# Kernel tuning notes

Measured on AMD Instinct MI355X. Metric: run time of the kernel, lower is better.

## Reference

```python
import jax, jax.numpy as jnp
import numpy as np
from jax import lax

NUM_MASKS = 100
NUM_CLASSES = 81  # 80 + 1
KERNEL_DIM = 256
BIAS_PRIOR = float(-np.log((1 - 0.01) / 0.01))


def setup_inputs() -> dict:
    key = jax.random.key(0)
    ks = jax.random.split(key, 12)
    B, C, H, W = 4, 256, 160, 160
    D = C  # expand_dim = in_channels * num_groups
    inp = {
        "features": jax.random.normal(ks[0], (B, C, H, W), jnp.float32),
        # iam_conv: Conv2d(C, num_masks, 3, padding=1)
        "w_iam": jax.random.normal(ks[1], (NUM_MASKS, C, 3, 3), jnp.float32) * 0.01,
        "b_iam": jnp.full((NUM_MASKS,), BIAS_PRIOR, jnp.float32),
        "softmax_bias": jnp.ones((1,), jnp.float32),
        # fc: Linear(D, D), xavier-ish
        "w_fc": jax.random.normal(ks[2], (D, D), jnp.float32) * (1.0 / np.sqrt(D)),
        "b_fc": jnp.zeros((D,), jnp.float32),
        "w_cls": jax.random.normal(ks[3], (NUM_CLASSES, D), jnp.float32) * 0.01,
        "b_cls": jnp.full((NUM_CLASSES,), BIAS_PRIOR, jnp.float32),
        "w_ker": jax.random.normal(ks[4], (KERNEL_DIM, D), jnp.float32) * 0.01,
        "b_ker": jnp.zeros((KERNEL_DIM,), jnp.float32),
        "w_obj": jax.random.normal(ks[5], (1, D), jnp.float32) * (1.0 / np.sqrt(D)),
        "b_obj": jnp.zeros((1,), jnp.float32),
        "w_box": jax.random.normal(ks[6], (4, D), jnp.float32) * 0.01,
        "b_box": jnp.zeros((4,), jnp.float32),
    }
    return inp


def reference(features, w_iam, b_iam, softmax_bias, w_fc, b_fc,
              w_cls, b_cls, w_ker, b_ker, w_obj, b_obj, w_box, b_box):
    B, C, H, W = features.shape
    # conv score map: (B, num_masks, H, W)
    iam = lax.conv_general_dilated(
        features, w_iam, window_strides=(1, 1), padding="SAME",
        dimension_numbers=("NCHW", "OIHW", "NCHW")) + b_iam[None, :, None, None]
    # num_groups == 1: single group iam
    iam_flat = iam.reshape(B, NUM_MASKS, H * W)
    # softmax over HW with learned scalar bias (bias shifts uniformly -> no-op math-wise but kept faithful)
    iam_prob = jax.nn.softmax(iam_flat + softmax_bias[0], axis=-1)  # (B, M, HW)
    # spatial attention pooling: bmm(prob, feats^T) -> (B, M, C)
    inst = jnp.einsum("bmp,bcp->bmc", iam_prob, features.reshape(B, C, H * W))
    # prev_inst_features is None -> skip fc_fuse
    inst = jax.nn.relu(inst @ w_fc.T + b_fc)
    pred_logits = inst @ w_cls.T + b_cls
    pred_kernel = inst @ w_ker.T + b_ker
    pred_scores = inst @ w_obj.T + b_obj
    pred_bboxes = inst @ w_box.T + b_box
    return (pred_logits, pred_kernel, pred_scores, pred_bboxes, iam, inst)
```

## Files before the change

kernel.cpp:

```cpp
#include <hip/hip_runtime.h>
#include <hip/hip_bf16.h>

typedef __attribute__((ext_vector_type(8))) short bf16x8;
typedef __attribute__((ext_vector_type(4))) float f32x4;

#define HW_ 25600
#define HP_ 162
#define WP_ 162

__device__ __forceinline__ unsigned short f2bf(float f) {
    union { float f; unsigned u; } x; x.f = f;
    unsigned r = x.u + 0x7FFFu + ((x.u >> 16) & 1u);
    return (unsigned short)(r >> 16);
}
__device__ __forceinline__ float bf2f(unsigned short v) {
    union { unsigned u; float f; } x; x.u = ((unsigned)v) << 16;
    return x.f;
}

typedef const __attribute__((address_space(1))) unsigned int* gas_t;
typedef __attribute__((address_space(3))) unsigned int* las_t;
__device__ __forceinline__ void gl_lds16(const void* g, void* l) {
    __builtin_amdgcn_global_load_lds((gas_t)g, (las_t)l, 16, 0, 0);
}

__global__ __launch_bounds__(256) void k_prep(const float* __restrict__ w_iam,
                                              unsigned short* __restrict__ wp,
                                              unsigned short* __restrict__ fpad) {
    int bid = blockIdx.x;
    if (bid < 1152) {
        int idx = bid * 256 + threadIdx.x;
        int stage = idx >> 12;
        int r = idx & 4095;
        int m = r >> 5, cl = r & 31;
        int tap = stage >> 3, kc = stage & 7;
        int jj = (cl >> 3) ^ ((m >> 1) & 3);
        int c = kc * 32 + jj * 8 + (cl & 7);
        int dy = (tap * 11) >> 5, dx = tap - dy * 3;
        float v = (m < 100) ? w_iam[((m * 256 + c) * 3 + dy) * 3 + dx] : 0.f;
        wp[idx] = f2bf(v);
    } else {
        int idx = (bid - 1152) * 256 + threadIdx.x;
        const int perb = 164864;
        if (idx >= 4 * perb) return;
        int b = idx / perb;
        int r = idx - b * perb;
        int hp, wpp, c;
        if (r < 82944) {
            hp = (r < 41472) ? 0 : 161;
            int r2 = r % 41472;
            wpp = r2 >> 8; c = r2 & 255;
        } else {
            r -= 82944;
            wpp = (r < 40960) ? 0 : 161;
            int r2 = r % 40960;
            hp = 1 + (r2 >> 8); c = r2 & 255;
        }
        fpad[((b * HP_ + hp) * WP_ + wpp) * 256 + c] = 0;
    }
}

__global__ __launch_bounds__(256) void k_convert(const float* __restrict__ feat,
                                                 unsigned short* __restrict__ fpad) {
    int bid = blockIdx.x;
    int b = bid / 640;
    int h = (bid >> 2) % 160;
    int c0 = (bid & 3) * 64;
    __shared__ float tile[64][161];
    int t = threadIdx.x;
    const float4* src4 = (const float4*)(feat + ((long)(b * 256 + c0) * 160 + h) * 160);
    #pragma unroll
    for (int s = 0; s < 10; ++s) {
        int q = t + s * 256;
        int ci = q / 40;
        int w4 = q - ci * 40;
        float4 v = src4[(long)ci * 6400 + w4];
        tile[ci][w4 * 4 + 0] = v.x;
        tile[ci][w4 * 4 + 1] = v.y;
        tile[ci][w4 * 4 + 2] = v.z;
        tile[ci][w4 * 4 + 3] = v.w;
    }
    __syncthreads();
    int co = (t & 7) * 8, wq = t >> 3;
    unsigned short* dst = fpad + ((long)(b * HP_ + h + 1) * WP_ + 1) * 256 + c0 + co;
    #pragma unroll
    for (int wp = 0; wp < 5; ++wp) {
        int w = wq + wp * 32;
        bf16x8 v;
        #pragma unroll
        for (int j = 0; j < 8; ++j) v[j] = (short)f2bf(tile[co + j][w]);
        *(bf16x8*)(dst + (long)w * 256) = v;
    }
}

__global__ __launch_bounds__(256, 3) void k_conv(const unsigned short* __restrict__ fpad,
                                                 const unsigned short* __restrict__ wprep,
                                                 const float* __restrict__ b_iam,
                                                 float* __restrict__ iam) {
    int bid = blockIdx.x;
    bid = (bid & 7) * 100 + (bid >> 3);
    int b = bid / 200;
    int p0 = (bid % 200) * 128;
    int tid = threadIdx.x;
    int lane = tid & 63, wid = tid >> 6;
    int wr = wid >> 1, wc = wid & 1;

    __shared__ __align__(16) char smem[24576 + 2 * 8448];

    int h0 = p0 / 160, w0 = p0 - h0 * 160;
    int istar = 160 - w0;
    const unsigned short* fb = fpad + (long)b * HP_ * WP_ * 256;

    long rterm[2];
    {
        int c = tid & 3;
        #pragma unroll
        for (int i = 0; i < 2; ++i) {
            int r = i * 64 + (tid >> 2);
            rterm[i] = (long)r * 256 + ((c ^ ((r >> 1) & 3)) << 3);
        }
    }
    long rterm2;
    {
        int r = 128 + ((lane & 15) >> 2), c = lane & 3;
        rterm2 = (long)r * 256 + ((c ^ ((r >> 1) & 3)) << 3);
    }

    f32x4 acc[4][4];
    #pragma unroll
    for (int i = 0; i < 4; ++i)
        #pragma unroll
        for (int j = 0; j < 4; ++j)
            #pragma unroll
            for (int k = 0; k < 4; ++k) acc[i][j][k] = 0.f;

    int aBase = (wr << 12) + ((lane & 15) << 6) + ((((lane >> 4) ^ ((lane >> 1) & 3))) << 4);
    int rb[4];
    #pragma unroll
    for (int nf = 0; nf < 4; ++nf) {
        int i = wc * 64 + nf * 16 + (lane & 15);
        rb[nf] = i + 2 * (i >= istar);
    }

    auto issueA = [&](int s) {
        int dy = s >> 3, kc = s & 7;
        #pragma unroll
        for (int dx = 0; dx < 3; ++dx) {
            const unsigned short* ga = wprep + ((long)((dy * 3 + dx) * 8 + kc) << 12) + (tid << 3);
            char* Adst = smem + (dx << 13) + (wid << 10);
            gl_lds16(ga, Adst);
            gl_lds16(ga + 2048, Adst + 4096);
        }
    };
    auto issueB = [&](int s, int bi) {
        int dy = s >> 3, kc = s & 7;
        char* Bd = smem + 24576 + bi * 8448;
        long base = ((long)((h0 + dy) * WP_ + w0)) * 256 + (kc << 5);
        gl_lds16(fb + base + rterm[0], Bd + (wid << 10));
        gl_lds16(fb + base + rterm[1], Bd + 4096 + (wid << 10));
        if (lane < 16) gl_lds16(fb + base + rterm2, Bd + 8192);
    };

    auto compute = [&](int bi) {
        const char* Ab = smem;
        const char* Bb = smem + 24576 + bi * 8448;
        #pragma unroll
        for (int dx = 0; dx < 3; ++dx) {
            bf16x8 af[4], bfv[4];
            #pragma unroll
            for (int mf = 0; mf < 4; ++mf)
                af[mf] = *(const bf16x8*)(Ab + (dx << 13) + aBase + (mf << 10));
            #pragma unroll
            for (int nf = 0; nf < 4; ++nf) {
                int row = rb[nf] + dx;
                bfv[nf] = *(const bf16x8*)(Bb + (row << 6) +
                            ((((lane >> 4) ^ ((row >> 1) & 3))) << 4));
            }
            __builtin_amdgcn_s_setprio(1);
            #pragma unroll
            for (int mf = 0; mf < 4; ++mf)
                #pragma unroll
                for (int nf = 0; nf < 4; ++nf)
                    acc[mf][nf] = __builtin_amdgcn_mfma_f32_16x16x32_bf16(
                        af[mf], bfv[nf], acc[mf][nf], 0, 0, 0);
            __builtin_amdgcn_s_setprio(0);
        }
    };

    issueB(0, 0);
    issueA(0);
    for (int s = 0; s < 24; ++s) {
        if (s < 23) {
            issueB(s + 1, (s + 1) & 1);
            asm volatile("s_waitcnt vmcnt(3)" ::: "memory");
        } else {
            asm volatile("s_waitcnt vmcnt(0)" ::: "memory");
        }
        __builtin_amdgcn_sched_barrier(0);
        __builtin_amdgcn_s_barrier();
        __builtin_amdgcn_sched_barrier(0);
        compute(s & 1);
        __builtin_amdgcn_sched_barrier(0);
        __builtin_amdgcn_s_barrier();
        __builtin_amdgcn_sched_barrier(0);
        if (s < 23) issueA(s + 1);
    }

    float* dst = iam + (long)b * 100 * HW_;
    #pragma unroll
    for (int mf = 0; mf < 4; ++mf)
        #pragma unroll
        for (int nf = 0; nf < 4; ++nf) {
            int p = p0 + wc * 64 + nf * 16 + (lane & 15);
            int m0 = wr * 64 + mf * 16 + ((lane >> 4) << 2);
            #pragma unroll
            for (int j = 0; j < 4; ++j) {
                int m = m0 + j;
                if (m < 100) dst[(long)m * HW_ + p] = acc[mf][nf][j] + b_iam[m];
            }
        }
}

__global__ __launch_bounds__(256, 2) void k_pool(const float* __restrict__ feat,
                                                 const float* __restrict__ iam,
                                                 unsigned short* __restrict__ partials,
                                                 float* __restrict__ psum) {
    int bid = blockIdx.x;
    int b = bid / 100;
    int sl = bid - b * 100;
    int p0 = sl * 256;
    int tid = threadIdx.x, lane = tid & 63, wq = tid >> 6;

    __shared__ __align__(16) unsigned short A[128 * 72];
    __shared__ __align__(16) unsigned short Bl[256 * 72];
    __shared__ float sums[128];
    if (tid < 128) sums[tid] = 0.f;
    __syncthreads();

    f32x4 acc[7][4];
    #pragma unroll
    for (int i = 0; i < 7; ++i)
        #pragma unroll
        for (int j = 0; j < 4; ++j)
            #pragma unroll
            for (int k = 0; k < 4; ++k) acc[i][j][k] = 0.f;

    int kgrp = (lane >> 4) << 3;

    for (int ks = 0; ks < 4; ++ks) {
        int k0 = p0 + ks * 64;
        for (int s = 0; s < 4; ++s) {
            int q = tid + s * 256;
            int mi = q >> 3, j0 = (q & 7) * 8;
            bf16x8 o;
            if (mi < 100) {
                const float4* sp4 = (const float4*)(iam + (long)(b * 100 + mi) * HW_ + k0 + j0);
                float4 v0 = sp4[0], v1 = sp4[1];
                float xv[8] = {v0.x, v0.y, v0.z, v0.w, v1.x, v1.y, v1.z, v1.w};
                float ls = 0.f;
                #pragma unroll
                for (int j = 0; j < 8; ++j) {
                    float e = __expf(xv[j]);
                    o[j] = (short)f2bf(e);
                    ls += e;
                }
                atomicAdd(&sums[mi], ls);
            } else {
                #pragma unroll
                for (int j = 0; j < 8; ++j) o[j] = 0;
            }
            *(bf16x8*)(A + mi * 72 + j0) = o;
        }
        for (int s = 0; s < 8; ++s) {
            int q = tid + s * 256;
            int ci = q >> 3, j0 = (q & 7) * 8;
            const float4* sp4 = (const float4*)(feat + (long)(b * 256 + ci) * HW_ + k0 + j0);
            float4 v0 = sp4[0], v1 = sp4[1];
            float xv[8] = {v0.x, v0.y, v0.z, v0.w, v1.x, v1.y, v1.z, v1.w};
            bf16x8 o;
            #pragma unroll
            for (int j = 0; j < 8; ++j) o[j] = (short)f2bf(xv[j]);
            *(bf16x8*)(Bl + ci * 72 + j0) = o;
        }
        __syncthreads();
        #pragma unroll
        for (int kk = 0; kk < 64; kk += 32) {
            bf16x8 af[7], bfv[4];
            #pragma unroll
            for (int mf = 0; mf < 7; ++mf)
                af[mf] = *(const bf16x8*)(A + (mf * 16 + (lane & 15)) * 72 + kk + kgrp);
            #pragma unroll
            for (int nf = 0; nf < 4; ++nf)
                bfv[nf] = *(const bf16x8*)(Bl + (wq * 64 + nf * 16 + (lane & 15)) * 72 + kk + kgrp);
            #pragma unroll
            for (int mf = 0; mf < 7; ++mf)
                #pragma unroll
                for (int nf = 0; nf < 4; ++nf)
                    acc[mf][nf] = __builtin_amdgcn_mfma_f32_16x16x32_bf16(
                        af[mf], bfv[nf], acc[mf][nf], 0, 0, 0);
        }
        __syncthreads();
    }
    if (tid < 100) psum[(long)bid * 112 + tid] = sums[tid];
    unsigned short* dst = partials + (long)bid * 112 * 256;
    #pragma unroll
    for (int mf = 0; mf < 7; ++mf)
        #pragma unroll
        for (int nf = 0; nf < 4; ++nf) {
            int m0 = mf * 16 + ((lane >> 4) << 2);
            int c  = wq * 64 + nf * 16 + (lane & 15);
            #pragma unroll
            for (int j = 0; j < 4; ++j)
                dst[(long)(m0 + j) * 256 + c] = f2bf(acc[mf][nf][j]);
        }
}

__global__ __launch_bounds__(256) void k_redfc(const unsigned short* __restrict__ partials,
                                               const float* __restrict__ psum,
                                               const float* __restrict__ w_fc, const float* __restrict__ b_fc,
                                               const float* __restrict__ w_cls, const float* __restrict__ b_cls,
                                               const float* __restrict__ w_ker, const float* __restrict__ b_ker,
                                               const float* __restrict__ w_obj, const float* __restrict__ b_obj,
                                               const float* __restrict__ w_box, const float* __restrict__ b_box,
                                               float* __restrict__ out) {
    int r = blockIdx.x;
    int b = r / 100, m = r - b * 100;
    int t = threadIdx.x;
    __shared__ float red[256];
    __shared__ float row[256];
    __shared__ float inst_s[256];

    red[t] = (t < 100) ? psum[(long)(b * 100 + t) * 112 + m] : 0.f;
    __syncthreads();
    for (int o = 128; o > 0; o >>= 1) {
        if (t < o) red[t] += red[t + o];
        __syncthreads();
    }
    float d = red[0];

    float s = 0.f;
    for (int sl = 0; sl < 100; ++sl)
        s += bf2f(partials[((long)(b * 100 + sl) * 112 + m) * 256 + t]);
    row[t] = s / d;
    __syncthreads();
    {
        float acc = b_fc[t];
        const float4* wv = (const float4*)(w_fc + (long)t * 256);
        for (int c = 0; c < 64; ++c) {
            float4 w4 = wv[c];
            acc += w4.x * row[c * 4] + w4.y * row[c * 4 + 1] + w4.z * row[c * 4 + 2] + w4.w * row[c * 4 + 3];
        }
        acc = fmaxf(acc, 0.f);
        inst_s[t] = acc;
        out[10376800 + (long)r * 256 + t] = acc;
    }
    __syncthreads();
    {
        float acc = b_ker[t];
        const float4* wv = (const float4*)(w_ker + (long)t * 256);
        for (int c = 0; c < 64; ++c) {
            float4 w4 = wv[c];
            acc += w4.x * inst_s[c * 4] + w4.y * inst_s[c * 4 + 1] + w4.z * inst_s[c * 4 + 2] + w4.w * inst_s[c * 4 + 3];
        }
        out[32400 + (long)r * 256 + t] = acc;
    }
    if (t < 81) {
        float acc = b_cls[t];
        const float4* wv = (const float4*)(w_cls + (long)t * 256);
        for (int c = 0; c < 64; ++c) {
            float4 w4 = wv[c];
            acc += w4.x * inst_s[c * 4] + w4.y * inst_s[c * 4 + 1] + w4.z * inst_s[c * 4 + 2] + w4.w * inst_s[c * 4 + 3];
        }
        out[(long)r * 81 + t] = acc;
    }
    if (t == 0) {
        float acc = b_obj[0];
        for (int c = 0; c < 256; ++c) acc += w_obj[c] * inst_s[c];
        out[134800 + r] = acc;
    }
    if (t >= 1 && t < 5) {
        int j = t - 1;
        float acc = b_box[j];
        for (int c = 0; c < 256; ++c) acc += w_box[j * 256 + c] * inst_s[c];
        out[135200 + (long)r * 4 + j] = acc;
    }
}

extern "C" void kernel_launch(void* const* d_in, const int* in_sizes, int n_in,
                              void* d_out, int out_size, void* d_ws, size_t ws_size,
                              hipStream_t stream) {
    const float* feat  = (const float*)d_in[0];
    const float* w_iam = (const float*)d_in[1];
    const float* b_iam = (const float*)d_in[2];
    const float* w_fc  = (const float*)d_in[4];
    const float* b_fc  = (const float*)d_in[5];
    const float* w_cls = (const float*)d_in[6];
    const float* b_cls = (const float*)d_in[7];
    const float* w_ker = (const float*)d_in[8];
    const float* b_ker = (const float*)d_in[9];
    const float* w_obj = (const float*)d_in[10];
    const float* b_obj = (const float*)d_in[11];
    const float* w_box = (const float*)d_in[12];
    const float* b_box = (const float*)d_in[13];
    float* out = (float*)d_out;

    char* ws = (char*)d_ws;
    unsigned short* fpad  = (unsigned short*)ws;
    unsigned short* wprep = (unsigned short*)(ws + 53747712);
    float* iam = out + 136800;

    unsigned short* partials = (unsigned short*)ws;
    float* psum              = (float*)(ws + 22937600);

    k_prep   <<<dim3(3728), dim3(256), 0, stream>>>(w_iam, wprep, fpad);
    k_convert<<<dim3(2560), dim3(256), 0, stream>>>(feat, fpad);
    k_conv   <<<dim3(800),  dim3(256), 0, stream>>>(fpad, wprep, b_iam, iam);
    k_pool   <<<dim3(400),  dim3(256), 0, stream>>>(feat, iam, partials, psum);
    k_redfc  <<<dim3(400),  dim3(256), 0, stream>>>(partials, psum, w_fc, b_fc, w_cls, b_cls,
                                                    w_ker, b_ker, w_obj, b_obj, w_box, b_box, out);
}
```

Baseline: 191.6 us.

## Widen conv tile to 256 pixels with 8 waves and merge prep/convert kernels

The conv kernel now uses 512-thread blocks, each covering 256 output pixels instead of 128. The weight (A) tile is shared by twice as many pixel columns, which halves weight loads per output and halves the block count. The B halo now spans two row wraps, and the wait counts are split per wave. The weight-prep, pad-zeroing and feature-conversion kernels are also fused into one launch to save launch overhead, but the larger LDS footprint and block size may reduce occupancy.

Result: faster. 173.2 us (median of 3 runs) (-9.6%).

```diff
diff --git a/kernel.cpp b/kernel.cpp
--- a/kernel.cpp
+++ b/kernel.cpp
@@ -24,9 +24,10 @@
     __builtin_amdgcn_global_load_lds((gas_t)g, (las_t)l, 16, 0, 0);
 }
 
-__global__ __launch_bounds__(256) void k_prep(const float* __restrict__ w_iam,
-                                              unsigned short* __restrict__ wp,
-                                              unsigned short* __restrict__ fpad) {
+__global__ __launch_bounds__(256) void k_prepcvt(const float* __restrict__ w_iam,
+                                                 unsigned short* __restrict__ wp,
+                                                 const float* __restrict__ feat,
+                                                 unsigned short* __restrict__ fpad) {
     int bid = blockIdx.x;
     if (bid < 1152) {
         int idx = bid * 256 + threadIdx.x;
@@ -39,7 +40,7 @@
         int dy = (tap * 11) >> 5, dx = tap - dy * 3;
         float v = (m < 100) ? w_iam[((m * 256 + c) * 3 + dy) * 3 + dx] : 0.f;
         wp[idx] = f2bf(v);
-    } else {
+    } else if (bid < 3728) {
         int idx = (bid - 1152) * 256 + threadIdx.x;
         const int perb = 164864;
         if (idx >= 4 * perb) return;
@@ -57,73 +58,67 @@
             hp = 1 + (r2 >> 8); c = r2 & 255;
         }
         fpad[((b * HP_ + hp) * WP_ + wpp) * 256 + c] = 0;
-    }
-}
-
-__global__ __launch_bounds__(256) void k_convert(const float* __restrict__ feat,
-                                                 unsigned short* __restrict__ fpad) {
-    int bid = blockIdx.x;
-    int b = bid / 640;
-    int h = (bid >> 2) % 160;
-    int c0 = (bid & 3) * 64;
-    __shared__ float tile[64][161];
-    int t = threadIdx.x;
-    const float4* src4 = (const float4*)(feat + ((long)(b * 256 + c0) * 160 + h) * 160);
-    #pragma unroll
-    for (int s = 0; s < 10; ++s) {
-        int q = t + s * 256;
-        int ci = q / 40;
-        int w4 = q - ci * 40;
-        float4 v = src4[(long)ci * 6400 + w4];
-        tile[ci][w4 * 4 + 0] = v.x;
-        tile[ci][w4 * 4 + 1] = v.y;
-        tile[ci][w4 * 4 + 2] = v.z;
-        tile[ci][w4 * 4 + 3] = v.w;
-    }
-    __syncthreads();
-    int co = (t & 7) * 8, wq = t >> 3;
-    unsigned short* dst = fpad + ((long)(b * HP_ + h + 1) * WP_ + 1) * 256 + c0 + co;
-    #pragma unroll
-    for (int wp = 0; wp < 5; ++wp) {
-        int w = wq + wp * 32;
-        bf16x8 v;
-        #pragma unroll
-        for (int j = 0; j < 8; ++j) v[j] = (short)f2bf(tile[co + j][w]);
-        *(bf16x8*)(dst + (long)w * 256) = v;
-    }
-}
-
-__global__ __launch_bounds__(256, 3) void k_conv(const unsigned short* __restrict__ fpad,
+    } else {
+        int cb = bid - 3728;
+        int b = cb / 640;
+        int h = (cb >> 2) % 160;
+        int c0 = (cb & 3) * 64;
+        __shared__ float tile[64][161];
+        int t = threadIdx.x;
+        const float4* src4 = (const float4*)(feat + ((long)(b * 256 + c0) * 160 + h) * 160);
+        #pragma unroll
+        for (int s = 0; s < 10; ++s) {
+            int q = t + s * 256;
+            int ci = q / 40;
+            int w4 = q - ci * 40;
+            float4 v = src4[(long)ci * 6400 + w4];
+            tile[ci][w4 * 4 + 0] = v.x;
+            tile[ci][w4 * 4 + 1] = v.y;
+            tile[ci][w4 * 4 + 2] = v.z;
+            tile[ci][w4 * 4 + 3] = v.w;
+        }
+        __syncthreads();
+        int co = (t & 7) * 8, wq = t >> 3;
+        unsigned short* dst = fpad + ((long)(b * HP_ + h + 1) * WP_ + 1) * 256 + c0 + co;
+        #pragma unroll
+        for (int wp2 = 0; wp2 < 5; ++wp2) {
+            int w = wq + wp2 * 32;
+            bf16x8 v;
+            #pragma unroll
+            for (int j = 0; j < 8; ++j) v[j] = (short)f2bf(tile[co + j][w]);
+            *(bf16x8*)(dst + (long)w * 256) = v;
+        }
+    }
+}
+
+__global__ __launch_bounds__(512, 4) void k_conv(const unsigned short* __restrict__ fpad,
                                                  const unsigned short* __restrict__ wprep,
                                                  const float* __restrict__ b_iam,
                                                  float* __restrict__ iam) {
     int bid = blockIdx.x;
-    bid = (bid & 7) * 100 + (bid >> 3);
-    int b = bid / 200;
-    int p0 = (bid % 200) * 128;
+    bid = (bid & 7) * 50 + (bid >> 3);
+    int b = bid / 100;
+    int p0 = (bid % 100) * 256;
     int tid = threadIdx.x;
     int lane = tid & 63, wid = tid >> 6;
-    int wr = wid >> 1, wc = wid & 1;
-
-    __shared__ __align__(16) char smem[24576 + 2 * 8448];
+    int wr = wid >> 2, wc = wid & 3;
+
+    __shared__ __align__(16) char smem[24576 + 2 * 17408];
 
     int h0 = p0 / 160, w0 = p0 - h0 * 160;
-    int istar = 160 - w0;
+    int istar1 = 160 - w0, istar2 = 320 - w0;
     const unsigned short* fb = fpad + (long)b * HP_ * WP_ * 256;
 
-    long rterm[2];
+    long rt0, rt1, rt2;
     {
         int c = tid & 3;
-        #pragma unroll
-        for (int i = 0; i < 2; ++i) {
-            int r = i * 64 + (tid >> 2);
-            rterm[i] = (long)r * 256 + ((c ^ ((r >> 1) & 3)) << 3);
-        }
-    }
-    long rterm2;
-    {
-        int r = 128 + ((lane & 15) >> 2), c = lane & 3;
-        rterm2 = (long)r * 256 + ((c ^ ((r >> 1) & 3)) << 3);
+        int r0 = tid >> 2;
+        rt0 = (long)r0 * 256 + ((c ^ ((r0 >> 1) & 3)) << 3);
+        int r1 = 128 + (tid >> 2);
+        rt1 = (long)r1 * 256 + ((c ^ ((r1 >> 1) & 3)) << 3);
+        int r2 = 256 + (lane >> 2);
+        int c2 = lane & 3;
+        rt2 = (long)r2 * 256 + ((c2 ^ ((r2 >> 1) & 3)) << 3);
     }
 
     f32x4 acc[4][4];
@@ -139,7 +134,7 @@
     #pragma unroll
     for (int nf = 0; nf < 4; ++nf) {
         int i = wc * 64 + nf * 16 + (lane & 15);
-        rb[nf] = i + 2 * (i >= istar);
+        rb[nf] = i + 2 * (i >= istar1) + 2 * (i >= istar2);
     }
 
     auto issueA = [&](int s) {
@@ -147,23 +142,21 @@
         #pragma unroll
         for (int dx = 0; dx < 3; ++dx) {
             const unsigned short* ga = wprep + ((long)((dy * 3 + dx) * 8 + kc) << 12) + (tid << 3);
-            char* Adst = smem + (dx << 13) + (wid << 10);
-            gl_lds16(ga, Adst);
-            gl_lds16(ga + 2048, Adst + 4096);
+            gl_lds16(ga, smem + (dx << 13) + (wid << 10));
         }
     };
     auto issueB = [&](int s, int bi) {
         int dy = s >> 3, kc = s & 7;
-        char* Bd = smem + 24576 + bi * 8448;
+        char* Bd = smem + 24576 + bi * 17408;
         long base = ((long)((h0 + dy) * WP_ + w0)) * 256 + (kc << 5);
-        gl_lds16(fb + base + rterm[0], Bd + (wid << 10));
-        gl_lds16(fb + base + rterm[1], Bd + 4096 + (wid << 10));
-        if (lane < 16) gl_lds16(fb + base + rterm2, Bd + 8192);
+        gl_lds16(fb + base + rt0, Bd + (wid << 10));
+        gl_lds16(fb + base + rt1, Bd + 8192 + (wid << 10));
+        if (wid == 0) gl_lds16(fb + base + rt2, Bd + 16384);
     };
 
     auto compute = [&](int bi) {
         const char* Ab = smem;
-        const char* Bb = smem + 24576 + bi * 8448;
+        const char* Bb = smem + 24576 + bi * 17408;
         #pragma unroll
         for (int dx = 0; dx < 3; ++dx) {
             bf16x8 af[4], bfv[4];
@@ -192,7 +185,8 @@
     for (int s = 0; s < 24; ++s) {
         if (s < 23) {
             issueB(s + 1, (s + 1) & 1);
-            asm volatile("s_waitcnt vmcnt(3)" ::: "memory");
+            if (wid == 0) asm volatile("s_waitcnt vmcnt(3)" ::: "memory");
+            else          asm volatile("s_waitcnt vmcnt(2)" ::: "memory");
         } else {
             asm volatile("s_waitcnt vmcnt(0)" ::: "memory");
         }
@@ -412,9 +406,8 @@
     unsigned short* partials = (unsigned short*)ws;
     float* psum              = (float*)(ws + 22937600);
 
-    k_prep   <<<dim3(3728), dim3(256), 0, stream>>>(w_iam, wprep, fpad);
-    k_convert<<<dim3(2560), dim3(256), 0, stream>>>(feat, fpad);
-    k_conv   <<<dim3(800),  dim3(256), 0, stream>>>(fpad, wprep, b_iam, iam);
+    k_prepcvt<<<dim3(6288), dim3(256), 0, stream>>>(w_iam, wprep, feat, fpad);
+    k_conv   <<<dim3(400),  dim3(512), 0, stream>>>(fpad, wprep, b_iam, iam);
     k_pool   <<<dim3(400),  dim3(256), 0, stream>>>(feat, iam, partials, psum);
     k_redfc  <<<dim3(400),  dim3(256), 0, stream>>>(partials, psum, w_fc, b_fc, w_cls, b_cls,
                                                     w_ker, b_ker, w_obj, b_obj, w_box, b_box, out);
```
